# Performance work log

Measured on AMD Instinct MI355X. Metric: run time of the kernel, lower is better.

Reference implementation:

```python
import jax, jax.numpy as jnp
import numpy as np

C_IN = 128
C_QK = C_IN // 8


def setup_inputs() -> dict:
    key = jax.random.key(0)
    kx, kq, kk, kv = jax.random.split(key, 4)
    x = jax.random.normal(kx, (8, C_IN, 64, 64), dtype=jnp.float32)
    # 1x1 conv weights, stored as (c_out, c_in); fan-in scaled init
    s = 1.0 / np.sqrt(C_IN)
    Wq = jax.random.normal(kq, (C_QK, C_IN), dtype=jnp.float32) * s
    Wk = jax.random.normal(kk, (C_QK, C_IN), dtype=jnp.float32) * s
    Wv = jax.random.normal(kv, (C_IN, C_IN), dtype=jnp.float32) * s
    gamma = jnp.ones((1,), dtype=jnp.float32) * 0.5  # nonzero so residual branch matters
    return {"x": x, "Wq": Wq, "Wk": Wk, "Wv": Wv, "gamma": gamma}


def reference(x, Wq, Wk, Wv, gamma):
    b, c, h, w = x.shape
    xt = rearr = x.reshape(b, c, h * w)            # b c n
    q = jnp.einsum('oc,bcn->bno', Wq, xt)          # b n c//8
    k = jnp.einsum('oc,bcn->bon', Wk, xt)          # b c//8 n
    v = jnp.einsum('oc,bcn->bno', Wv, xt)          # b n c
    energy = jnp.einsum('bno,bom->bnm', q, k)      # b n n (no scale, per source)
    attn = jax.nn.softmax(energy, axis=-1)
    out = jnp.einsum('bnm,bmc->bnc', attn, v)      # b n c
    out = out.transpose(0, 2, 1).reshape(b, c, h, w)
    return x + gamma[0] * out
```

## Files before the change

### kernel.cpp

```cpp
#include <hip/hip_runtime.h>
#include <hip/hip_bf16.h>


typedef __bf16 bf16x8 __attribute__((ext_vector_type(8)));
typedef __bf16 bf16x4 __attribute__((ext_vector_type(4)));
typedef float  f32x16 __attribute__((ext_vector_type(16)));

static constexpr int Bb = 8, Cc = 128, Nn = 4096, CQ = 16;

__device__ __forceinline__ f32x16 mfma32(bf16x8 a, bf16x8 b, f32x16 c) {
    return __builtin_amdgcn_mfma_f32_32x32x16_bf16(a, b, c, 0, 0, 0);
}
struct HL { __bf16 h, l; };
__device__ __forceinline__ HL hilo(float f) {
    HL r;
    r.h = (__bf16)f;
    r.l = (__bf16)(f - (float)r.h);
    return r;
}

__global__ __launch_bounds__(256) void qkv_kernel(
    const float* __restrict__ x, const float* __restrict__ Wq,
    const float* __restrict__ Wk, const float* __restrict__ Wv,
    float* __restrict__ qw, float* __restrict__ kw, __bf16* __restrict__ vw)
{
    const int b = blockIdx.y, n0 = blockIdx.x * 64, t = threadIdx.x;
    const int wave = t >> 6, lane = t & 63, lr = lane & 31, lq = lane >> 5;

    __shared__ __bf16 xh[64][136], xl[64][136];
    __shared__ __bf16 wqh[32][136], wql[32][136];
    __shared__ __bf16 wvh[128][136];

    {
        const int n = t & 63, cib = t >> 6;
        #pragma unroll 4
        for (int i = 0; i < 32; ++i) {
            int ci = cib + i * 4;
            float v = x[((size_t)(b * Cc + ci)) * Nn + n0 + n];
            HL z = hilo(v);
            xh[n][ci] = z.h; xl[n][ci] = z.l;
        }
    }
    #pragma unroll
    for (int i = 0; i < 8; ++i) {
        int idx = t + i * 256;
        int o = idx >> 7, ci = idx & 127;
        HL zq = hilo(Wq[idx]);
        wqh[o][ci] = zq.h; wql[o][ci] = zq.l;
        HL zk = hilo(Wk[idx]);
        wqh[16 + o][ci] = zk.h; wql[16 + o][ci] = zk.l;
    }
    #pragma unroll
    for (int i = 0; i < 16; ++i) {
        int flat = t * 4 + i * 1024;
        float4 w4 = *(const float4*)(Wv + flat);
        int c = flat >> 7, ci0 = flat & 127;
        bf16x4 h4 = { (__bf16)w4.x, (__bf16)w4.y, (__bf16)w4.z, (__bf16)w4.w };
        *(bf16x4*)&wvh[c][ci0] = h4;
    }
    __syncthreads();

    if (wave < 2) {
        const int nh = wave;
        f32x16 acc = {};
        #pragma unroll
        for (int ks = 0; ks < 8; ++ks) {
            bf16x8 ah = *(const bf16x8*)&wqh[lr][ks * 16 + lq * 8];
            bf16x8 al = *(const bf16x8*)&wql[lr][ks * 16 + lq * 8];
            bf16x8 bh = *(const bf16x8*)&xh[nh * 32 + lr][ks * 16 + lq * 8];
            bf16x8 bl = *(const bf16x8*)&xl[nh * 32 + lr][ks * 16 + lq * 8];
            acc = mfma32(ah, bh, acc);
            acc = mfma32(al, bh, acc);
            acc = mfma32(ah, bl, acc);
        }
        const int n = n0 + nh * 32 + lr;
        #pragma unroll
        for (int r = 0; r < 16; ++r) {
            int op = (r & 3) + 8 * (r >> 2) + 4 * lq;
            if (op < 16) qw[((size_t)(b * Nn + n)) * CQ + op] = acc[r];
            else         kw[((size_t)(b * Nn + n)) * CQ + (op - 16)] = acc[r];
        }
    }
    {
        int tl[3][2]; int nt;
        if      (wave == 0) { tl[0][0]=2; tl[0][1]=0; nt=1; }
        else if (wave == 1) { tl[0][0]=2; tl[0][1]=1; nt=1; }
        else if (wave == 2) { tl[0][0]=0; tl[0][1]=0; tl[1][0]=1; tl[1][1]=0; tl[2][0]=3; tl[2][1]=0; nt=3; }
        else                { tl[0][0]=0; tl[0][1]=1; tl[1][0]=1; tl[1][1]=1; tl[2][0]=3; tl[2][1]=1; nt=3; }
        for (int ti = 0; ti < nt; ++ti) {
            const int ct = tl[ti][0], nh = tl[ti][1];
            f32x16 acc = {};
            #pragma unroll
            for (int ks = 0; ks < 8; ++ks) {
                bf16x8 a  = *(const bf16x8*)&wvh[ct * 32 + lr][ks * 16 + lq * 8];
                bf16x8 bh = *(const bf16x8*)&xh[nh * 32 + lr][ks * 16 + lq * 8];
                acc = mfma32(a, bh, acc);
            }
            const int n = n0 + nh * 32 + lr;
            #pragma unroll
            for (int r = 0; r < 16; ++r) {
                int c = (r & 3) + 8 * (r >> 2) + 4 * lq + ct * 32;
                vw[((size_t)(b * Cc + c)) * Nn + n] = (__bf16)acc[r];
            }
        }
    }
}

__global__ __launch_bounds__(256) void attn_kernel(
    const float* __restrict__ x, const float* __restrict__ qw,
    const float* __restrict__ kw, const __bf16* __restrict__ vw,
    const float* __restrict__ gamma, float* __restrict__ out)
{
    const int b = blockIdx.y, n0b = blockIdx.x * 128, t = threadIdx.x;
    const int wave = t >> 6, lane = t & 63, lr = lane & 31, lq = lane >> 5;

    __shared__ __bf16 qT[128][40];
    __shared__ __bf16 kT[64][40];
    __shared__ __bf16 vT[128][72];
    __shared__ __bf16 Pl[4][32][72];

    #pragma unroll
    for (int i = 0; i < 2; ++i) {
        int idx = t + i * 256;
        int n = idx >> 2, og = idx & 3;
        float4 q4 = *(const float4*)(qw + ((size_t)(b * Nn + n0b + n)) * CQ + og * 4);
        HL z0 = hilo(q4.x), z1 = hilo(q4.y), z2 = hilo(q4.z), z3 = hilo(q4.w);
        bf16x4 h = { z0.h, z1.h, z2.h, z3.h };
        bf16x4 l = { z0.l, z1.l, z2.l, z3.l };
        *(bf16x4*)&qT[n][og * 4] = h;
        *(bf16x4*)&qT[n][16 + og * 4] = l;
    }

    const int vc = t >> 3, vs = t & 7;
    const int kr = t >> 2, kg = t & 3;
    uint4 vreg[4]; float4 kreg;

    auto load_chunk = [&](int m0) {
        #pragma unroll
        for (int i = 0; i < 4; ++i)
            vreg[i] = *(const uint4*)(vw + ((size_t)(b * Cc + vc + 32 * i)) * Nn + m0 + vs * 8);
        kreg = *(const float4*)(kw + ((size_t)(b * Nn + m0 + kr)) * CQ + kg * 4);
    };
    auto store_chunk = [&]() {
        #pragma unroll
        for (int i = 0; i < 4; ++i)
            *(uint4*)&vT[vc + 32 * i][vs * 8] = vreg[i];
        HL z0 = hilo(kreg.x), z1 = hilo(kreg.y), z2 = hilo(kreg.z), z3 = hilo(kreg.w);
        bf16x4 h = { z0.h, z1.h, z2.h, z3.h };
        bf16x4 l = { z0.l, z1.l, z2.l, z3.l };
        *(bf16x4*)&kT[kr][kg * 4] = h;
        *(bf16x4*)&kT[kr][16 + kg * 4] = l;
    };

    load_chunk(0);
    store_chunk();
    __syncthreads();

    const bf16x8 qhi = *(const bf16x8*)&qT[wave * 32 + lr][lq * 8];
    const bf16x8 qlo = *(const bf16x8*)&qT[wave * 32 + lr][16 + lq * 8];

    f32x16 acc[4] = {{}, {}, {}, {}};
    float m_run = -3e38f, l_run = 0.f;

    for (int it = 0; it < 64; ++it) {
        load_chunk((it < 63 ? it + 1 : 63) * 64);

        f32x16 s0 = {}, s1 = {};
        {
            bf16x8 kh = *(const bf16x8*)&kT[lr][lq * 8];
            bf16x8 kl = *(const bf16x8*)&kT[lr][16 + lq * 8];
            s0 = mfma32(kh, qhi, s0); s0 = mfma32(kl, qhi, s0); s0 = mfma32(kh, qlo, s0);
            kh = *(const bf16x8*)&kT[32 + lr][lq * 8];
            kl = *(const bf16x8*)&kT[32 + lr][16 + lq * 8];
            s1 = mfma32(kh, qhi, s1); s1 = mfma32(kl, qhi, s1); s1 = mfma32(kh, qlo, s1);
        }

        float cmax = -3e38f;
        #pragma unroll
        for (int r = 0; r < 16; ++r) { cmax = fmaxf(cmax, s0[r]); cmax = fmaxf(cmax, s1[r]); }
        cmax = fmaxf(cmax, __shfl_xor(cmax, 32));
        const float mnew = fmaxf(m_run, cmax);
        const float alpha = __expf(m_run - mnew);
        float p0[16], p1[16], csum = 0.f;
        #pragma unroll
        for (int r = 0; r < 16; ++r) {
            p0[r] = __expf(s0[r] - mnew); csum += p0[r];
            p1[r] = __expf(s1[r] - mnew); csum += p1[r];
        }
        csum += __shfl_xor(csum, 32);
        l_run = l_run * alpha + csum;
        m_run = mnew;
        #pragma unroll
        for (int ct = 0; ct < 4; ++ct)
            #pragma unroll
            for (int r = 0; r < 16; ++r) acc[ct][r] *= alpha;

        #pragma unroll
        for (int g = 0; g < 4; ++g) {
            bf16x4 a = { (__bf16)p0[4*g], (__bf16)p0[4*g+1], (__bf16)p0[4*g+2], (__bf16)p0[4*g+3] };
            *(bf16x4*)&Pl[wave][lr][lq * 4 + g * 8] = a;
            bf16x4 c4 = { (__bf16)p1[4*g], (__bf16)p1[4*g+1], (__bf16)p1[4*g+2], (__bf16)p1[4*g+3] };
            *(bf16x4*)&Pl[wave][lr][32 + lq * 4 + g * 8] = c4;
        }

        bf16x8 pf[4];
        #pragma unroll
        for (int ks = 0; ks < 4; ++ks)
            pf[ks] = *(const bf16x8*)&Pl[wave][lr][ks * 16 + lq * 8];
        #pragma unroll
        for (int ct = 0; ct < 4; ++ct) {
            #pragma unroll
            for (int ks = 0; ks < 4; ++ks) {
                bf16x8 va = *(const bf16x8*)&vT[ct * 32 + lr][ks * 16 + lq * 8];
                acc[ct] = mfma32(va, pf[ks], acc[ct]);
            }
        }

        __syncthreads();
        store_chunk();
        __syncthreads();
    }

    const float g = gamma[0];
    const float linv = 1.0f / l_run;
    const int n = n0b + wave * 32 + lr;
    #pragma unroll
    for (int ct = 0; ct < 4; ++ct) {
        #pragma unroll
        for (int r = 0; r < 16; ++r) {
            int c = (r & 3) + 8 * (r >> 2) + 4 * lq + ct * 32;
            size_t idx = ((size_t)(b * Cc + c)) * Nn + n;
            out[idx] = x[idx] + g * acc[ct][r] * linv;
        }
    }
}

extern "C" void kernel_launch(void* const* d_in, const int* in_sizes, int n_in,
                              void* d_out, int out_size, void* d_ws, size_t ws_size,
                              hipStream_t stream) {
    const float* x  = (const float*)d_in[0];
    const float* Wq = (const float*)d_in[1];
    const float* Wk = (const float*)d_in[2];
    const float* Wv = (const float*)d_in[3];
    const float* gm = (const float*)d_in[4];

    float* qw = (float*)d_ws;
    float* kw = qw + (size_t)Bb * Nn * CQ;
    __bf16* vw = (__bf16*)(kw + (size_t)Bb * Nn * CQ);

    qkv_kernel<<<dim3(Nn / 64, Bb), 256, 0, stream>>>(x, Wq, Wk, Wv, qw, kw, vw);
    attn_kernel<<<dim3(Nn / 128, Bb), 256, 0, stream>>>(x, qw, kw, vw, gm,
                                                        (float*)d_out);
}
```

Baseline: 224.2 us.

## Split keys across waves, drop online max, read K/V straight from global

The attention kernel now gives each block 32 queries and splits the 4096 keys across its four waves. Each wave streams K and V straight from global memory into registers, with no LDS staging and no per-iteration barriers. Partial accumulators are combined at the end through LDS atomics. Softmax no longer tracks a running max: Q is pre-scaled by log2(e) and raw exp2 is used, which removes the rescaling work but can overflow if energies grow large. The QKV kernel stops staging Wv in shared memory and converts it from global per MFMA step; the P fragment is built with cross-lane shuffles instead of an LDS round-trip.

```diff
diff --git a/kernel.cpp b/kernel.cpp
--- a/kernel.cpp
+++ b/kernel.cpp
@@ -17,6 +17,11 @@
     r.h = (__bf16)f;
     r.l = (__bf16)(f - (float)r.h);
     return r;
+}
+__device__ __forceinline__ unsigned int pack2bf(float a, float b) {
+    union { __bf16 h[2]; unsigned int u; } x;
+    x.h[0] = (__bf16)a; x.h[1] = (__bf16)b;
+    return x.u;
 }
 
 __global__ __launch_bounds__(256) void qkv_kernel(
@@ -29,7 +34,6 @@
 
     __shared__ __bf16 xh[64][136], xl[64][136];
     __shared__ __bf16 wqh[32][136], wql[32][136];
-    __shared__ __bf16 wvh[128][136];
 
     {
         const int n = t & 63, cib = t >> 6;
@@ -50,14 +54,6 @@
         HL zk = hilo(Wk[idx]);
         wqh[16 + o][ci] = zk.h; wql[16 + o][ci] = zk.l;
     }
-    #pragma unroll
-    for (int i = 0; i < 16; ++i) {
-        int flat = t * 4 + i * 1024;
-        float4 w4 = *(const float4*)(Wv + flat);
-        int c = flat >> 7, ci0 = flat & 127;
-        bf16x4 h4 = { (__bf16)w4.x, (__bf16)w4.y, (__bf16)w4.z, (__bf16)w4.w };
-        *(bf16x4*)&wvh[c][ci0] = h4;
-    }
     __syncthreads();
 
     if (wave < 2) {
@@ -77,7 +73,7 @@
         #pragma unroll
         for (int r = 0; r < 16; ++r) {
             int op = (r & 3) + 8 * (r >> 2) + 4 * lq;
-            if (op < 16) qw[((size_t)(b * Nn + n)) * CQ + op] = acc[r];
+            if (op < 16) qw[((size_t)(b * Nn + n)) * CQ + op] = acc[r] * 1.44269504089f;
             else         kw[((size_t)(b * Nn + n)) * CQ + (op - 16)] = acc[r];
         }
     }
@@ -92,7 +88,11 @@
             f32x16 acc = {};
             #pragma unroll
             for (int ks = 0; ks < 8; ++ks) {
-                bf16x8 a  = *(const bf16x8*)&wvh[ct * 32 + lr][ks * 16 + lq * 8];
+                const float* wp = Wv + (ct * 32 + lr) * Cc + ks * 16 + lq * 8;
+                float4 w0 = *(const float4*)wp;
+                float4 w1 = *(const float4*)(wp + 4);
+                bf16x8 a = { (__bf16)w0.x, (__bf16)w0.y, (__bf16)w0.z, (__bf16)w0.w,
+                             (__bf16)w1.x, (__bf16)w1.y, (__bf16)w1.z, (__bf16)w1.w };
                 bf16x8 bh = *(const bf16x8*)&xh[nh * 32 + lr][ks * 16 + lq * 8];
                 acc = mfma32(a, bh, acc);
             }
@@ -106,132 +106,129 @@
     }
 }
 
-__global__ __launch_bounds__(256) void attn_kernel(
+__global__ __launch_bounds__(256, 3) void attn_kernel(
     const float* __restrict__ x, const float* __restrict__ qw,
     const float* __restrict__ kw, const __bf16* __restrict__ vw,
     const float* __restrict__ gamma, float* __restrict__ out)
 {
-    const int b = blockIdx.y, n0b = blockIdx.x * 128, t = threadIdx.x;
+    const int h = blockIdx.x;
+    const int b = h & 7;
+    const int n0 = (h >> 3) * 32;
+    const int t = threadIdx.x;
     const int wave = t >> 6, lane = t & 63, lr = lane & 31, lq = lane >> 5;
 
-    __shared__ __bf16 qT[128][40];
-    __shared__ __bf16 kT[64][40];
-    __shared__ __bf16 vT[128][72];
-    __shared__ __bf16 Pl[4][32][72];
-
+    __shared__ float accbuf[32][129];
+    __shared__ float lbuf[32];
+
+    bf16x8 qhi, qlo;
+    {
+        const float* qp = qw + ((size_t)(b * Nn + n0 + lr)) * CQ + lq * 8;
+        float4 q0 = *(const float4*)qp;
+        float4 q1 = *(const float4*)(qp + 4);
+        HL z0 = hilo(q0.x), z1 = hilo(q0.y), z2 = hilo(q0.z), z3 = hilo(q0.w);
+        HL z4 = hilo(q1.x), z5 = hilo(q1.y), z6 = hilo(q1.z), z7 = hilo(q1.w);
+        qhi = (bf16x8){ z0.h, z1.h, z2.h, z3.h, z4.h, z5.h, z6.h, z7.h };
+        qlo = (bf16x8){ z0.l, z1.l, z2.l, z3.l, z4.l, z5.l, z6.l, z7.l };
+    }
+
+    const float* kbase = kw + ((size_t)(b * Nn + lr)) * CQ + lq * 8;
+    const __bf16* vbs[4];
     #pragma unroll
-    for (int i = 0; i < 2; ++i) {
-        int idx = t + i * 256;
-        int n = idx >> 2, og = idx & 3;
-        float4 q4 = *(const float4*)(qw + ((size_t)(b * Nn + n0b + n)) * CQ + og * 4);
-        HL z0 = hilo(q4.x), z1 = hilo(q4.y), z2 = hilo(q4.z), z3 = hilo(q4.w);
-        bf16x4 h = { z0.h, z1.h, z2.h, z3.h };
-        bf16x4 l = { z0.l, z1.l, z2.l, z3.l };
-        *(bf16x4*)&qT[n][og * 4] = h;
-        *(bf16x4*)&qT[n][16 + og * 4] = l;
-    }
-
-    const int vc = t >> 3, vs = t & 7;
-    const int kr = t >> 2, kg = t & 3;
-    uint4 vreg[4]; float4 kreg;
-
-    auto load_chunk = [&](int m0) {
-        #pragma unroll
-        for (int i = 0; i < 4; ++i)
-            vreg[i] = *(const uint4*)(vw + ((size_t)(b * Cc + vc + 32 * i)) * Nn + m0 + vs * 8);
-        kreg = *(const float4*)(kw + ((size_t)(b * Nn + m0 + kr)) * CQ + kg * 4);
-    };
-    auto store_chunk = [&]() {
-        #pragma unroll
-        for (int i = 0; i < 4; ++i)
-            *(uint4*)&vT[vc + 32 * i][vs * 8] = vreg[i];
-        HL z0 = hilo(kreg.x), z1 = hilo(kreg.y), z2 = hilo(kreg.z), z3 = hilo(kreg.w);
-        bf16x4 h = { z0.h, z1.h, z2.h, z3.h };
-        bf16x4 l = { z0.l, z1.l, z2.l, z3.l };
-        *(bf16x4*)&kT[kr][kg * 4] = h;
-        *(bf16x4*)&kT[kr][16 + kg * 4] = l;
-    };
-
-    load_chunk(0);
-    store_chunk();
+    for (int ct = 0; ct < 4; ++ct)
+        vbs[ct] = vw + ((size_t)(b * Cc + ct * 32 + lr)) * Nn + lq * 8;
+
+    f32x16 acc[4] = {{}, {}, {}, {}};
+    float l_part = 0.f;
+    const int kw0 = wave * 1024;
+
+    for (int it = 0; it < 32; ++it) {
+        const int m0 = kw0 + it * 32;
+
+        float4 ka = *(const float4*)(kbase + (size_t)m0 * CQ);
+        float4 kb = *(const float4*)(kbase + (size_t)m0 * CQ + 4);
+        bf16x8 vf[4][2];
+        #pragma unroll
+        for (int ct = 0; ct < 4; ++ct) {
+            vf[ct][0] = *(const bf16x8*)(vbs[ct] + m0);
+            vf[ct][1] = *(const bf16x8*)(vbs[ct] + m0 + 16);
+        }
+
+        bf16x8 khi, klo;
+        {
+            HL z0 = hilo(ka.x), z1 = hilo(ka.y), z2 = hilo(ka.z), z3 = hilo(ka.w);
+            HL z4 = hilo(kb.x), z5 = hilo(kb.y), z6 = hilo(kb.z), z7 = hilo(kb.w);
+            khi = (bf16x8){ z0.h, z1.h, z2.h, z3.h, z4.h, z5.h, z6.h, z7.h };
+            klo = (bf16x8){ z0.l, z1.l, z2.l, z3.l, z4.l, z5.l, z6.l, z7.l };
+        }
+
+        f32x16 s = {};
+        s = mfma32(khi, qhi, s);
+        s = mfma32(klo, qhi, s);
+        s = mfma32(khi, qlo, s);
+
+        float p[16];
+        #pragma unroll
+        for (int r = 0; r < 16; ++r) p[r] = __builtin_amdgcn_exp2f(s[r]);
+        l_part += ((((p[0] + p[1]) + (p[2] + p[3])) + ((p[4] + p[5]) + (p[6] + p[7])))
+                 + (((p[8] + p[9]) + (p[10] + p[11])) + ((p[12] + p[13]) + (p[14] + p[15]))));
+
+        unsigned int G00 = pack2bf(p[0],  p[1]),  G01 = pack2bf(p[2],  p[3]);
+        unsigned int G10 = pack2bf(p[4],  p[5]),  G11 = pack2bf(p[6],  p[7]);
+        unsigned int G20 = pack2bf(p[8],  p[9]),  G21 = pack2bf(p[10], p[11]);
+        unsigned int G30 = pack2bf(p[12], p[13]), G31 = pack2bf(p[14], p[15]);
+
+        unsigned int sA0 = lq ? G00 : G10, sA1 = lq ? G01 : G11;
+        unsigned int sB0 = lq ? G20 : G30, sB1 = lq ? G21 : G31;
+        unsigned int rA0 = __shfl_xor(sA0, 32), rA1 = __shfl_xor(sA1, 32);
+        unsigned int rB0 = __shfl_xor(sB0, 32), rB1 = __shfl_xor(sB1, 32);
+
+        union U8 { unsigned int u[4]; bf16x8 v; };
+        U8 f0, f1;
+        f0.u[0] = lq ? rA0 : G00;  f0.u[1] = lq ? rA1 : G01;
+        f0.u[2] = lq ? G10 : rA0;  f0.u[3] = lq ? G11 : rA1;
+        f1.u[0] = lq ? rB0 : G20;  f1.u[1] = lq ? rB1 : G21;
+        f1.u[2] = lq ? G30 : rB0;  f1.u[3] = lq ? G31 : rB1;
+
+        #pragma unroll
+        for (int ct = 0; ct < 4; ++ct) {
+            acc[ct] = mfma32(vf[ct][0], f0.v, acc[ct]);
+            acc[ct] = mfma32(vf[ct][1], f1.v, acc[ct]);
+        }
+    }
+
+    l_part += __shfl_xor(l_part, 32);
+
+    if (wave == 0) {
+        #pragma unroll
+        for (int ct = 0; ct < 4; ++ct)
+            #pragma unroll
+            for (int r = 0; r < 16; ++r) {
+                int c = (r & 3) + 8 * (r >> 2) + 4 * lq + 32 * ct;
+                accbuf[lr][c] = acc[ct][r];
+            }
+        if (lane < 32) lbuf[lr] = l_part;
+    }
     __syncthreads();
-
-    const bf16x8 qhi = *(const bf16x8*)&qT[wave * 32 + lr][lq * 8];
-    const bf16x8 qlo = *(const bf16x8*)&qT[wave * 32 + lr][16 + lq * 8];
-
-    f32x16 acc[4] = {{}, {}, {}, {}};
-    float m_run = -3e38f, l_run = 0.f;
-
-    for (int it = 0; it < 64; ++it) {
-        load_chunk((it < 63 ? it + 1 : 63) * 64);
-
-        f32x16 s0 = {}, s1 = {};
-        {
-            bf16x8 kh = *(const bf16x8*)&kT[lr][lq * 8];
-            bf16x8 kl = *(const bf16x8*)&kT[lr][16 + lq * 8];
-            s0 = mfma32(kh, qhi, s0); s0 = mfma32(kl, qhi, s0); s0 = mfma32(kh, qlo, s0);
-            kh = *(const bf16x8*)&kT[32 + lr][lq * 8];
-            kl = *(const bf16x8*)&kT[32 + lr][16 + lq * 8];
-            s1 = mfma32(kh, qhi, s1); s1 = mfma32(kl, qhi, s1); s1 = mfma32(kh, qlo, s1);
-        }
-
-        float cmax = -3e38f;
-        #pragma unroll
-        for (int r = 0; r < 16; ++r) { cmax = fmaxf(cmax, s0[r]); cmax = fmaxf(cmax, s1[r]); }
-        cmax = fmaxf(cmax, __shfl_xor(cmax, 32));
-        const float mnew = fmaxf(m_run, cmax);
-        const float alpha = __expf(m_run - mnew);
-        float p0[16], p1[16], csum = 0.f;
-        #pragma unroll
-        for (int r = 0; r < 16; ++r) {
-            p0[r] = __expf(s0[r] - mnew); csum += p0[r];
-            p1[r] = __expf(s1[r] - mnew); csum += p1[r];
-        }
-        csum += __shfl_xor(csum, 32);
-        l_run = l_run * alpha + csum;
-        m_run = mnew;
+    if (wave != 0) {
         #pragma unroll
         for (int ct = 0; ct < 4; ++ct)
             #pragma unroll
-            for (int r = 0; r < 16; ++r) acc[ct][r] *= alpha;
-
-        #pragma unroll
-        for (int g = 0; g < 4; ++g) {
-            bf16x4 a = { (__bf16)p0[4*g], (__bf16)p0[4*g+1], (__bf16)p0[4*g+2], (__bf16)p0[4*g+3] };
-            *(bf16x4*)&Pl[wave][lr][lq * 4 + g * 8] = a;
-            bf16x4 c4 = { (__bf16)p1[4*g], (__bf16)p1[4*g+1], (__bf16)p1[4*g+2], (__bf16)p1[4*g+3] };
-            *(bf16x4*)&Pl[wave][lr][32 + lq * 4 + g * 8] = c4;
-        }
-
-        bf16x8 pf[4];
-        #pragma unroll
-        for (int ks = 0; ks < 4; ++ks)
-            pf[ks] = *(const bf16x8*)&Pl[wave][lr][ks * 16 + lq * 8];
-        #pragma unroll
-        for (int ct = 0; ct < 4; ++ct) {
-            #pragma unroll
-            for (int ks = 0; ks < 4; ++ks) {
-                bf16x8 va = *(const bf16x8*)&vT[ct * 32 + lr][ks * 16 + lq * 8];
-                acc[ct] = mfma32(va, pf[ks], acc[ct]);
-            }
-        }
-
-        __syncthreads();
-        store_chunk();
-        __syncthreads();
-    }
+            for (int r = 0; r < 16; ++r) {
+                int c = (r & 3) + 8 * (r >> 2) + 4 * lq + 32 * ct;
+                atomicAdd(&accbuf[lr][c], acc[ct][r]);
+            }
+        if (lane < 32) atomicAdd(&lbuf[lr], l_part);
+    }
+    __syncthreads();
 
     const float g = gamma[0];
-    const float linv = 1.0f / l_run;
-    const int n = n0b + wave * 32 + lr;
+    const int q = t & 31, c0 = t >> 5;
+    const float linv = 1.0f / lbuf[q];
     #pragma unroll
-    for (int ct = 0; ct < 4; ++ct) {
-        #pragma unroll
-        for (int r = 0; r < 16; ++r) {
-            int c = (r & 3) + 8 * (r >> 2) + 4 * lq + ct * 32;
-            size_t idx = ((size_t)(b * Cc + c)) * Nn + n;
-            out[idx] = x[idx] + g * acc[ct][r] * linv;
-        }
+    for (int i = 0; i < 16; ++i) {
+        int c = c0 + 8 * i;
+        size_t idx = ((size_t)(b * Cc + c)) * Nn + n0 + q;
+        out[idx] = x[idx] + g * accbuf[q][c] * linv;
     }
 }
 
@@ -249,6 +246,6 @@
     __bf16* vw = (__bf16*)(kw + (size_t)Bb * Nn * CQ);
 
     qkv_kernel<<<dim3(Nn / 64, Bb), 256, 0, stream>>>(x, Wq, Wk, Wv, qw, kw, vw);
-    attn_kernel<<<dim3(Nn / 128, Bb), 256, 0, stream>>>(x, qw, kw, vw, gm,
+    attn_kernel<<<dim3(Nn / 32 * Bb), 256, 0, stream>>>(x, qw, kw, vw, gm,
                                                         (float*)d_out);
 }
```

Measured after the change: 278.7 us. 1.24x slower.
